# Kernel optimization log

Hardware: AMD Instinct MI355X
Metric: run time of the kernel (lower is better)

The kernel has to match this reference:

```python
import jax, jax.numpy as jnp
import numpy as np

N, M, E, C, F, K = 10000, 20000, 160000, 128, 128, 3
R_CORRECTION = 1.0  # UpsampleModule passes 1 to DPOConv


def setup_inputs() -> dict:
    key = jax.random.key(0)
    ks = jax.random.split(key, 8)
    x = jax.random.normal(ks[0], (N, C), dtype=jnp.float32)
    pos = jax.random.uniform(ks[1], (N, 2), dtype=jnp.float32)
    pos_skip = jax.random.uniform(ks[2], (M, 2), dtype=jnp.float32)
    edge_index = jax.random.randint(ks[3], (2, E), 0, N, dtype=jnp.int64)
    W_conv = jax.random.normal(ks[4], (4 * C, F), dtype=jnp.float32) * 0.02
    b_conv = jnp.zeros((F,), dtype=jnp.float32)
    W2 = jax.random.normal(ks[5], (F, F), dtype=jnp.float32) * 0.02
    b2 = jnp.zeros((F,), dtype=jnp.float32)
    return {"x": x, "pos": pos, "pos_skip": pos_skip, "edge_index": edge_index,
            "W_conv": W_conv, "b_conv": b_conv, "W2": W2, "b2": b2}


def _dpo_conv(x, pos, edge_index, W_conv, b_conv):
    src, dst = edge_index[0], edge_index[1]  # PyG flow: j=source, i=target
    v_j, v_i = x[src], x[dst]                # [E, C]
    diff = pos[dst] - pos[src]               # pos_i - pos_j, [E, 2]
    r2 = jnp.sum(diff * diff, axis=-1)       # [E]
    scale = R_CORRECTION / (r2 + 0.01)       # [E]
    dx = diff[:, 0] * scale
    dy = diff[:, 1] * scale
    v_diff = v_i - v_j
    f = jnp.concatenate([v_diff * dx[:, None], v_diff * dy[:, None], v_j], axis=1)  # [E, 3C]
    agg = jax.ops.segment_sum(f, dst, num_segments=N)
    cnt = jax.ops.segment_sum(jnp.ones((E,), x.dtype), dst, num_segments=N)
    agg = agg / jnp.maximum(cnt, 1.0)[:, None]  # aggr='mean'
    h = jnp.concatenate([agg, x], axis=1) @ W_conv + b_conv  # [N, F]
    return h


def _knn_interpolate(h, pos, pos_skip, k):
    # squared distances target->source, [M, N]
    d2 = jnp.sum((pos_skip[:, None, :] - pos[None, :, :]) ** 2, axis=-1)
    neg_d, idx = jax.lax.top_k(-d2, k)         # k nearest, [M, k]
    w = 1.0 / jnp.maximum(-neg_d, 1e-16)       # inverse squared-distance weights
    return jnp.sum(w[:, :, None] * h[idx], axis=1) / jnp.sum(w, axis=1)[:, None]


def reference(x, pos, pos_skip, edge_index, W_conv, b_conv, W2, b2):
    h = _dpo_conv(x, pos, edge_index, W_conv, b_conv)
    h = jax.nn.elu(h)
    h = jax.nn.elu(h @ W2 + b2)
    return _knn_interpolate(h, pos, pos_skip, K)  # [M, F]
```

## Files before the change

kernel.cpp:

```cpp
#include <hip/hip_runtime.h>
#include <hip/hip_bf16.h>
#include <math.h>
#include <float.h>
#include <stdint.h>

#define N_NODES 10000
#define M_PTS   20000
#define E_EDGES 160000
#define C_CH    128
#define F_CH    128
#define G_GRID  64
#define N_CELLS (G_GRID*G_GRID)
#define NPB     16
#define ECAP    64
#define CCAP    24
#define AROWS   10048
#define GROWS   64
#define S_STRIDE 136
#define N_TILES (N_NODES / NPB)
#define W1SZ (4*C_CH*F_CH)
#define W2SZ (F_CH*F_CH)

typedef __attribute__((ext_vector_type(8))) short short8;
typedef __attribute__((ext_vector_type(4))) float f32x4;

__device__ inline ushort f2bf(float v) {
    __hip_bfloat16 b = __float2bfloat16(v);
    return *reinterpret_cast<ushort*>(&b);
}
__device__ inline float bf2f(ushort u) {
    __hip_bfloat16 b = *reinterpret_cast<__hip_bfloat16*>(&u);
    return __bfloat162float(b);
}
__device__ inline float eluf(float v) { return (v > 0.f) ? v : expm1f(v); }
__device__ inline void insert3(uint64_t key, uint64_t& k0, uint64_t& k1, uint64_t& k2) {
    bool lt2 = key < k2, lt1 = key < k1, lt0 = key < k0;
    k2 = lt1 ? k1 : (lt2 ? key : k2);
    k1 = lt0 ? k0 : (lt1 ? key : k1);
    k0 = lt0 ? key : k0;
}

__global__ __launch_bounds__(256) void build_kernel(const int* __restrict__ ei,
    const float* __restrict__ pos, int* __restrict__ ecur, int* __restrict__ ccur,
    int4* __restrict__ edata, int4* __restrict__ cdata,
    const float* __restrict__ Wc, const float* __restrict__ W2,
    ushort* __restrict__ Wct_h, ushort* __restrict__ Wct_l,
    ushort* __restrict__ W2t_h, ushort* __restrict__ W2t_l)
{
    int i = blockIdx.x * 256 + threadIdx.x;
    if (i < E_EDGES) {
        int src = ei[i];
        int dst = ei[E_EDGES + i];
        float dxv = pos[2*dst]     - pos[2*src];
        float dyv = pos[2*dst + 1] - pos[2*src + 1];
        float r2 = dxv*dxv + dyv*dyv;
        float scale = 1.0f / (r2 + 0.01f);
        int slot = atomicAdd(&ecur[dst], 1);
        if (slot < ECAP)
            edata[dst*ECAP + slot] = make_int4(src, __float_as_int(dxv*scale),
                                               __float_as_int(dyv*scale), 0);
    } else if (i < E_EDGES + N_NODES) {
        int j = i - E_EDGES;
        float px = pos[2*j], py = pos[2*j+1];
        int cx = min(max((int)(px * G_GRID), 0), G_GRID - 1);
        int cy = min(max((int)(py * G_GRID), 0), G_GRID - 1);
        int c = cy * G_GRID + cx;
        int slot = atomicAdd(&ccur[c], 1);
        if (slot < CCAP)
            cdata[c*CCAP + slot] = make_int4(__float_as_int(px), __float_as_int(py), j, 0);
    } else if (i < E_EDGES + N_NODES + W1SZ) {
        int j = i - (E_EDGES + N_NODES);
        int n = j >> 9, k = j & 511;
        float v = Wc[k*F_CH + n];
        ushort h = f2bf(v);
        Wct_h[j] = h;
        Wct_l[j] = f2bf(v - bf2f(h));
    } else if (i < E_EDGES + N_NODES + W1SZ + W2SZ) {
        int j = i - (E_EDGES + N_NODES + W1SZ);
        int n = j >> 7, k = j & 127;
        float v = W2[k*F_CH + n];
        ushort h = f2bf(v);
        W2t_h[j] = h;
        W2t_l[j] = f2bf(v - bf2f(h));
    }
}

__global__ __launch_bounds__(1024, 8) void mega_kernel(const float* __restrict__ x,
    const int* __restrict__ ecur, const int4* __restrict__ edata,
    ushort* __restrict__ Ah, ushort* __restrict__ Al,
    const float* __restrict__ pos_skip, const int* __restrict__ ccur,
    const int4* __restrict__ cdata,
    int* __restrict__ knn_idx, float* __restrict__ knn_w)
{
    const int bid = blockIdx.x;
    const int tid = threadIdx.x;
    const int lane = tid & 63;
    const int wave = tid >> 6;

    if (bid % 5 == 4) {
        int gt = (bid / 5) * 1024 + tid;
        if (gt >= M_PTS * 8) return;
        int t = gt >> 3;
        int sub = gt & 7;
        float tx = pos_skip[2*t], ty = pos_skip[2*t+1];
        const float h = 1.0f / G_GRID;
        int cx = min(max((int)(tx * G_GRID), 0), G_GRID - 1);
        int cy = min(max((int)(ty * G_GRID), 0), G_GRID - 1);

        uint64_t m0 = UINT64_MAX, m1 = UINT64_MAX, m2 = UINT64_MAX;
        bool done;
        {
            uint64_t k0 = UINT64_MAX, k1 = UINT64_MAX, k2 = UINT64_MAX;
            int cc[4];
            int qq[4];
            #pragma unroll
            for (int s = 0; s < 4; s++) {
                int cidx = sub + 8*s;
                int yy = cy + cidx / 5 - 2;
                int xx = cx + cidx % 5 - 2;
                bool ok = (cidx < 25) && (yy >= 0) && (yy < G_GRID) &&
                          (xx >= 0) && (xx < G_GRID);
                cc[s] = ok ? (yy * G_GRID + xx) : -1;
            }
            #pragma unroll
            for (int s = 0; s < 4; s++)
                qq[s] = (cc[s] >= 0) ? min(ccur[cc[s]], CCAP) : 0;
            #pragma unroll
            for (int s = 0; s < 4; s++) {
                const int4* cb = cdata + (size_t)(cc[s] < 0 ? 0 : cc[s]) * CCAP;
                int q = qq[s];
                int p = 0;
                for (; p + 1 < q; p += 2) {
                    int4 sa = cb[p];
                    int4 sb = cb[p+1];
                    float dax = __fadd_rn(__int_as_float(sa.x), -tx);
                    float day = __fadd_rn(__int_as_float(sa.y), -ty);
                    float da  = __fadd_rn(__fmul_rn(dax, dax), __fmul_rn(day, day));
                    insert3(((uint64_t)__float_as_uint(da) << 32) | (uint32_t)sa.z, k0, k1, k2);
                    float dbx = __fadd_rn(__int_as_float(sb.x), -tx);
                    float dby = __fadd_rn(__int_as_float(sb.y), -ty);
                    float db  = __fadd_rn(__fmul_rn(dbx, dbx), __fmul_rn(dby, dby));
                    insert3(((uint64_t)__float_as_uint(db) << 32) | (uint32_t)sb.z, k0, k1, k2);
                }
                if (p < q) {
                    int4 sa = cb[p];
                    float dax = __fadd_rn(__int_as_float(sa.x), -tx);
                    float day = __fadd_rn(__int_as_float(sa.y), -ty);
                    float da  = __fadd_rn(__fmul_rn(dax, dax), __fmul_rn(day, day));
                    insert3(((uint64_t)__float_as_uint(da) << 32) | (uint32_t)sa.z, k0, k1, k2);
                }
            }
            m0 = k0; m1 = k1; m2 = k2;
            #pragma unroll
            for (int m = 1; m <= 4; m <<= 1) {
                uint64_t p0 = __shfl_xor((unsigned long long)m0, m, 64);
                uint64_t p1 = __shfl_xor((unsigned long long)m1, m, 64);
                uint64_t p2 = __shfl_xor((unsigned long long)m2, m, 64);
                insert3(p0, m0, m1, m2);
                insert3(p1, m0, m1, m2);
                insert3(p2, m0, m1, m2);
            }
            float d2cur = __uint_as_float((uint32_t)(m2 >> 32));
            done = (d2cur < (2.0f * h) * (2.0f * h) * 0.99999f);
        }

        if (!done) {
            uint64_t k0 = UINT64_MAX, k1 = UINT64_MAX, k2 = UINT64_MAX;
            m0 = UINT64_MAX; m1 = UINT64_MAX; m2 = UINT64_MAX;
            for (int r = 0; ; r++) {
                if (r >= 2) {
                    m0 = k0; m1 = k1; m2 = k2;
                    #pragma unroll
                    for (int m = 1; m <= 4; m <<= 1) {
                        uint64_t p0 = __shfl_xor((unsigned long long)m0, m, 64);
                        uint64_t p1 = __shfl_xor((unsigned long long)m1, m, 64);
                        uint64_t p2 = __shfl_xor((unsigned long long)m2, m, 64);
                        insert3(p0, m0, m1, m2);
                        insert3(p1, m0, m1, m2);
                        insert3(p2, m0, m1, m2);
                    }
                    float bound = ((r - 1) * h) * ((r - 1) * h) * 0.99999f;
                    float d2cur = __uint_as_float((uint32_t)(m2 >> 32));
                    if (d2cur < bound || r >= G_GRID) break;
                }
                int x0 = max(cx - r, 0), x1 = min(cx + r, G_GRID - 1);
                int y0 = max(cy - r, 0), y1 = min(cy + r, G_GRID - 1);
                int cidx = 0;
                for (int yy = y0; yy <= y1; yy++) {
                    bool yedge = (yy == cy - r) || (yy == cy + r);
                    for (int xx = x0; xx <= x1; xx++) {
                        if (r > 0 && !yedge && xx != cx - r && xx != cx + r) continue;
                        if ((cidx++ & 7) != sub) continue;
                        int c = yy * G_GRID + xx;
                        int pc = min(ccur[c], CCAP);
                        const int4* cb = cdata + c*CCAP;
                        for (int p = 0; p < pc; p++) {
                            int4 sp = cb[p];
                            float ddx = __fadd_rn(__int_as_float(sp.x), -tx);
                            float ddy = __fadd_rn(__int_as_float(sp.y), -ty);
                            float dd = __fadd_rn(__fmul_rn(ddx, ddx), __fmul_rn(ddy, ddy));
                            uint64_t key = ((uint64_t)__float_as_uint(dd) << 32) | (uint32_t)sp.z;
                            insert3(key, k0, k1, k2);
                        }
                    }
                }
            }
        }

        if (sub == 0) {
            float d0 = __uint_as_float((uint32_t)(m0 >> 32));
            float d1 = __uint_as_float((uint32_t)(m1 >> 32));
            float d2 = __uint_as_float((uint32_t)(m2 >> 32));
            float w0 = 1.0f / fmaxf(d0, 1e-16f);
            float w1 = 1.0f / fmaxf(d1, 1e-16f);
            float w2 = 1.0f / fmaxf(d2, 1e-16f);
            float wsum = w0 + w1 + w2;
            knn_idx[t*3+0] = (int)(uint32_t)m0;
            knn_idx[t*3+1] = (int)(uint32_t)m1;
            knn_idx[t*3+2] = (int)(uint32_t)m2;
            knn_w[t*3+0] = w0 / wsum;
            knn_w[t*3+1] = w1 / wsum;
            knn_w[t*3+2] = w2 / wsum;
        }
        return;
    }

    const int agg_id = bid - bid / 5;
    if (agg_id >= N_TILES) return;
    const int nodeBase = agg_id * NPB;
    const float2* xv = (const float2*)x;

    {
        const int rr = wave;
        int node = nodeBase + rr;
        float2 xi = xv[(size_t)node*64 + lane];
        int cnt = ecur[node];
        int m = min(cnt, ECAP);
        int4 er = make_int4(0, 0, 0, 0);
        if (lane < m)
            er = edata[(size_t)node*ECAP + lane];
        double a1x = 0., a1y = 0., a2x = 0., a2y = 0., a3x = 0., a3y = 0.;
        int p = 0;
        for (; p + 7 < m; p += 8) {
            int s0 = __shfl(er.x, p);     int s1 = __shfl(er.x, p+1);
            int s2 = __shfl(er.x, p+2);   int s3 = __shfl(er.x, p+3);
            int s4 = __shfl(er.x, p+4);   int s5 = __shfl(er.x, p+5);
            int s6 = __shfl(er.x, p+6);   int s7 = __shfl(er.x, p+7);
            float dx0 = __int_as_float(__shfl(er.y, p));
            float dy0 = __int_as_float(__shfl(er.z, p));
            float dx1 = __int_as_float(__shfl(er.y, p+1));
            float dy1 = __int_as_float(__shfl(er.z, p+1));
            float dx2 = __int_as_float(__shfl(er.y, p+2));
            float dy2 = __int_as_float(__shfl(er.z, p+2));
            float dx3 = __int_as_float(__shfl(er.y, p+3));
            float dy3 = __int_as_float(__shfl(er.z, p+3));
            float dx4 = __int_as_float(__shfl(er.y, p+4));
            float dy4 = __int_as_float(__shfl(er.z, p+4));
            float dx5 = __int_as_float(__shfl(er.y, p+5));
            float dy5 = __int_as_float(__shfl(er.z, p+5));
            float dx6 = __int_as_float(__shfl(er.y, p+6));
            float dy6 = __int_as_float(__shfl(er.z, p+6));
            float dx7 = __int_as_float(__shfl(er.y, p+7));
            float dy7 = __int_as_float(__shfl(er.z, p+7));
            float2 x0 = xv[(size_t)s0*64 + lane];
            float2 x1 = xv[(size_t)s1*64 + lane];
            float2 x2 = xv[(size_t)s2*64 + lane];
            float2 x3 = xv[(size_t)s3*64 + lane];
            float2 x4 = xv[(size_t)s4*64 + lane];
            float2 x5 = xv[(size_t)s5*64 + lane];
            float2 x6 = xv[(size_t)s6*64 + lane];
            float2 x7 = xv[(size_t)s7*64 + lane];
            a1x += (double)((xi.x-x0.x)*dx0); a1y += (double)((xi.y-x0.y)*dx0);
            a2x += (double)((xi.x-x0.x)*dy0); a2y += (double)((xi.y-x0.y)*dy0);
            a3x += (double)x0.x;              a3y += (double)x0.y;
            a1x += (double)((xi.x-x1.x)*dx1); a1y += (double)((xi.y-x1.y)*dx1);
            a2x += (double)((xi.x-x1.x)*dy1); a2y += (double)((xi.y-x1.y)*dy1);
            a3x += (double)x1.x;              a3y += (double)x1.y;
            a1x += (double)((xi.x-x2.x)*dx2); a1y += (double)((xi.y-x2.y)*dx2);
            a2x += (double)((xi.x-x2.x)*dy2); a2y += (double)((xi.y-x2.y)*dy2);
            a3x += (double)x2.x;              a3y += (double)x2.y;
            a1x += (double)((xi.x-x3.x)*dx3); a1y += (double)((xi.y-x3.y)*dx3);
            a2x += (double)((xi.x-x3.x)*dy3); a2y += (double)((xi.y-x3.y)*dy3);
            a3x += (double)x3.x;              a3y += (double)x3.y;
            a1x += (double)((xi.x-x4.x)*dx4); a1y += (double)((xi.y-x4.y)*dx4);
            a2x += (double)((xi.x-x4.x)*dy4); a2y += (double)((xi.y-x4.y)*dy4);
            a3x += (double)x4.x;              a3y += (double)x4.y;
            a1x += (double)((xi.x-x5.x)*dx5); a1y += (double)((xi.y-x5.y)*dx5);
            a2x += (double)((xi.x-x5.x)*dy5); a2y += (double)((xi.y-x5.y)*dy5);
            a3x += (double)x5.x;              a3y += (double)x5.y;
            a1x += (double)((xi.x-x6.x)*dx6); a1y += (double)((xi.y-x6.y)*dx6);
            a2x += (double)((xi.x-x6.x)*dy6); a2y += (double)((xi.y-x6.y)*dy6);
            a3x += (double)x6.x;              a3y += (double)x6.y;
            a1x += (double)((xi.x-x7.x)*dx7); a1y += (double)((xi.y-x7.y)*dx7);
            a2x += (double)((xi.x-x7.x)*dy7); a2y += (double)((xi.y-x7.y)*dy7);
            a3x += (double)x7.x;              a3y += (double)x7.y;
        }
        for (; p + 3 < m; p += 4) {
            int s0 = __shfl(er.x, p);     int s1 = __shfl(er.x, p+1);
            int s2 = __shfl(er.x, p+2);   int s3 = __shfl(er.x, p+3);
            float dx0 = __int_as_float(__shfl(er.y, p));
            float dy0 = __int_as_float(__shfl(er.z, p));
            float dx1 = __int_as_float(__shfl(er.y, p+1));
            float dy1 = __int_as_float(__shfl(er.z, p+1));
            float dx2 = __int_as_float(__shfl(er.y, p+2));
            float dy2 = __int_as_float(__shfl(er.z, p+2));
            float dx3 = __int_as_float(__shfl(er.y, p+3));
            float dy3 = __int_as_float(__shfl(er.z, p+3));
            float2 x0 = xv[(size_t)s0*64 + lane];
            float2 x1 = xv[(size_t)s1*64 + lane];
            float2 x2 = xv[(size_t)s2*64 + lane];
            float2 x3 = xv[(size_t)s3*64 + lane];
            a1x += (double)((xi.x-x0.x)*dx0); a1y += (double)((xi.y-x0.y)*dx0);
            a2x += (double)((xi.x-x0.x)*dy0); a2y += (double)((xi.y-x0.y)*dy0);
            a3x += (double)x0.x;              a3y += (double)x0.y;
            a1x += (double)((xi.x-x1.x)*dx1); a1y += (double)((xi.y-x1.y)*dx1);
            a2x += (double)((xi.x-x1.x)*dy1); a2y += (double)((xi.y-x1.y)*dy1);
            a3x += (double)x1.x;              a3y += (double)x1.y;
            a1x += (double)((xi.x-x2.x)*dx2); a1y += (double)((xi.y-x2.y)*dx2);
            a2x += (double)((xi.x-x2.x)*dy2); a2y += (double)((xi.y-x2.y)*dy2);
            a3x += (double)x2.x;              a3y += (double)x2.y;
            a1x += (double)((xi.x-x3.x)*dx3); a1y += (double)((xi.y-x3.y)*dx3);
            a2x += (double)((xi.x-x3.x)*dy3); a2y += (double)((xi.y-x3.y)*dy3);
            a3x += (double)x3.x;              a3y += (double)x3.y;
        }
        for (; p < m; p++) {
            int s = __shfl(er.x, p);
            float dxe = __int_as_float(__shfl(er.y, p));
            float dye = __int_as_float(__shfl(er.z, p));
            float2 xj = xv[(size_t)s*64 + lane];
            float vx = xi.x - xj.x, vy = xi.y - xj.y;
            a1x += (double)(vx*dxe); a1y += (double)(vy*dxe);
            a2x += (double)(vx*dye); a2y += (double)(vy*dye);
            a3x += (double)xj.x;     a3y += (double)xj.y;
        }
        float inv = 1.0f / fmaxf((float)cnt, 1.0f);
        float vals[4][2] = {{(float)a1x*inv, (float)a1y*inv},
                            {(float)a2x*inv, (float)a2y*inv},
                            {(float)a3x*inv, (float)a3y*inv},
                            {xi.x, xi.y}};
        uint* Ah32 = (uint*)Ah;
        uint* Al32 = (uint*)Al;
        size_t b32 = (size_t)node*256;
        #pragma unroll
        for (int seg = 0; seg < 4; seg++) {
            ushort hx = f2bf(vals[seg][0]), hy = f2bf(vals[seg][1]);
            ushort lx = f2bf(vals[seg][0] - bf2f(hx)), ly = f2bf(vals[seg][1] - bf2f(hy));
            Ah32[b32 + seg*64 + lane] = (uint)hx | ((uint)hy << 16);
            Al32[b32 + seg*64 + lane] = (uint)lx | ((uint)ly << 16);
        }
    }
}

__global__ __launch_bounds__(512) void gemm_kernel(
    const ushort* __restrict__ Ah, const ushort* __restrict__ Al,
    const ushort* __restrict__ Wct_h, const ushort* __restrict__ Wct_l,
    const ushort* __restrict__ W2t_h, const ushort* __restrict__ W2t_l,
    const float* __restrict__ bc, const float* __restrict__ b2,
    float* __restrict__ h2out)
{
    __shared__ alignas(16) ushort sP0[GROWS * S_STRIDE];
    __shared__ alignas(16) ushort sP1[GROWS * S_STRIDE];

    const int tid   = threadIdx.x;
    const int lane  = tid & 63;
    const int wave  = tid >> 6;
    const int col16 = lane & 15;
    const int quad  = lane >> 4;
    const int ncol  = wave*16 + col16;
    const int rowBase = blockIdx.x * GROWS;

    const float bcv = bc[ncol];
    f32x4 acc0 = {0,0,0,0}, acc1 = {0,0,0,0}, acc2 = {0,0,0,0}, acc3 = {0,0,0,0};

    const int srow = tid >> 3;
    const int sseg = tid & 7;

    for (int kc = 0; kc < 4; kc++) {
        if (kc) __syncthreads();
        {
            size_t g = (size_t)(rowBase + srow)*512 + kc*128 + sseg*16;
            int l = srow*S_STRIDE + sseg*16;
            *(short8*)&sP0[l]     = *(const short8*)&Ah[g];
            *(short8*)&sP0[l + 8] = *(const short8*)&Ah[g + 8];
            *(short8*)&sP1[l]     = *(const short8*)&Al[g];
            *(short8*)&sP1[l + 8] = *(const short8*)&Al[g + 8];
        }
        __syncthreads();
        for (int ks = 0; ks < 4; ks++) {
            int kb = ks*32 + quad*8;
            short8 bh = *(const short8*)(Wct_h + (size_t)ncol*512 + kc*128 + kb);
            short8 bl = *(const short8*)(Wct_l + (size_t)ncol*512 + kc*128 + kb);
            #pragma unroll
            for (int rt = 0; rt < 4; rt++) {
                int ar = (rt*16 + col16)*S_STRIDE + kb;
                short8 ah = *(const short8*)&sP0[ar];
                short8 al = *(const short8*)&sP1[ar];
                f32x4 a = (rt==0)?acc0:(rt==1)?acc1:(rt==2)?acc2:acc3;
                a = __builtin_amdgcn_mfma_f32_16x16x32_bf16(ah, bh, a, 0, 0, 0);
                a = __builtin_amdgcn_mfma_f32_16x16x32_bf16(ah, bl, a, 0, 0, 0);
                a = __builtin_amdgcn_mfma_f32_16x16x32_bf16(al, bh, a, 0, 0, 0);
                if (rt==0) acc0 = a; else if (rt==1) acc1 = a; else if (rt==2) acc2 = a; else acc3 = a;
            }
        }
    }
    __syncthreads();

    #pragma unroll
    for (int rt = 0; rt < 4; rt++) {
        f32x4 a = (rt==0)?acc0:(rt==1)?acc1:(rt==2)?acc2:acc3;
        #pragma unroll
        for (int r = 0; r < 4; r++) {
            int row = rt*16 + quad*4 + r;
            float v = eluf(a[r] + bcv);
            ushort hh = f2bf(v);
            sP0[row*S_STRIDE + ncol] = hh;
            sP1[row*S_STRIDE + ncol] = f2bf(v - bf2f(hh));
        }
    }
    __syncthreads();

    const float b2v = b2[ncol];
    f32x4 c0 = {0,0,0,0}, c1 = {0,0,0,0}, c2 = {0,0,0,0}, c3 = {0,0,0,0};
    for (int ks = 0; ks < 4; ks++) {
        int kb = ks*32 + quad*8;
        short8 bh = *(const short8*)(W2t_h + ncol*128 + kb);
        short8 bl = *(const short8*)(W2t_l + ncol*128 + kb);
        #pragma unroll
        for (int rt = 0; rt < 4; rt++) {
            int ar = (rt*16 + col16)*S_STRIDE + kb;
            short8 ah = *(const short8*)&sP0[ar];
            short8 al = *(const short8*)&sP1[ar];
            f32x4 a = (rt==0)?c0:(rt==1)?c1:(rt==2)?c2:c3;
            a = __builtin_amdgcn_mfma_f32_16x16x32_bf16(ah, bh, a, 0, 0, 0);
            a = __builtin_amdgcn_mfma_f32_16x16x32_bf16(ah, bl, a, 0, 0, 0);
            a = __builtin_amdgcn_mfma_f32_16x16x32_bf16(al, bh, a, 0, 0, 0);
            if (rt==0) c0 = a; else if (rt==1) c1 = a; else if (rt==2) c2 = a; else c3 = a;
        }
    }
    #pragma unroll
    for (int rt = 0; rt < 4; rt++) {
        f32x4 a = (rt==0)?c0:(rt==1)?c1:(rt==2)?c2:c3;
        #pragma unroll
        for (int r = 0; r < 4; r++) {
            int node = rowBase + rt*16 + quad*4 + r;
            if (node < N_NODES)
                h2out[(size_t)node*F_CH + ncol] = eluf(a[r] + b2v);
        }
    }
}

__global__ __launch_bounds__(256) void gather_kernel(const float* __restrict__ h2,
    const int* __restrict__ knn_idx, const float* __restrict__ knn_w,
    float* __restrict__ out)
{
    int m = blockIdx.x * 4 + (threadIdx.x >> 6);
    int lane = threadIdx.x & 63;
    const float2* h2v = (const float2*)h2;
    int j0 = knn_idx[m*3+0], j1 = knn_idx[m*3+1], j2 = knn_idx[m*3+2];
    float w0 = knn_w[m*3+0], w1 = knn_w[m*3+1], w2 = knn_w[m*3+2];
    float2 a = h2v[(size_t)j0*64 + lane], b = h2v[(size_t)j1*64 + lane], c = h2v[(size_t)j2*64 + lane];
    float2 v;
    v.x = w0*a.x + w1*b.x + w2*c.x;
    v.y = w0*a.y + w1*b.y + w2*c.y;
    ((float2*)out)[(size_t)m*64 + lane] = v;
}

extern "C" void kernel_launch(void* const* d_in, const int* in_sizes, int n_in,
                              void* d_out, int out_size, void* d_ws, size_t ws_size,
                              hipStream_t stream) {
    const float* x        = (const float*)d_in[0];
    const float* pos      = (const float*)d_in[1];
    const float* pos_skip = (const float*)d_in[2];
    const int*   ei       = (const int*)  d_in[3];
    const float* Wc       = (const float*)d_in[4];
    const float* bc       = (const float*)d_in[5];
    const float* W2       = (const float*)d_in[6];
    const float* b2       = (const float*)d_in[7];
    float* out = (float*)d_out;

    char* ws = (char*)d_ws;
    size_t off = 0;
    auto alloc = [&](size_t bytes) {
        void* p = ws + off;
        off = (off + bytes + 255) & ~(size_t)255;
        return p;
    };
    int*    ecur    = (int*)   alloc((size_t)N_NODES * 4);
    int*    ccur    = (int*)   alloc((size_t)N_CELLS * 4);
    size_t  cur_bytes = (size_t)((char*)ccur - (char*)ecur) + (size_t)N_CELLS * 4;
    int4*   edata   = (int4*)  alloc((size_t)N_NODES * ECAP * 16);
    int4*   cdata   = (int4*)  alloc((size_t)N_CELLS * CCAP * 16);
    float*  h2      = (float*) alloc((size_t)N_NODES * F_CH * 4);
    int*    knn_idx = (int*)   alloc((size_t)M_PTS * 3 * 4);
    float*  knn_w   = (float*) alloc((size_t)M_PTS * 3 * 4);
    ushort* Wct_h   = (ushort*)alloc((size_t)F_CH * 512 * 2);
    ushort* Wct_l   = (ushort*)alloc((size_t)F_CH * 512 * 2);
    ushort* W2t_h   = (ushort*)alloc((size_t)F_CH * 128 * 2);
    ushort* W2t_l   = (ushort*)alloc((size_t)F_CH * 128 * 2);
    ushort* Ah      = (ushort*)alloc((size_t)AROWS * 512 * 2);
    ushort* Al      = (ushort*)alloc((size_t)AROWS * 512 * 2);

    hipMemsetAsync(ecur, 0, cur_bytes, stream);
    const int TOT = E_EDGES + N_NODES + W1SZ + W2SZ;
    build_kernel<<<(TOT + 255) / 256, 256, 0, stream>>>(ei, pos, ecur, ccur, edata, cdata,
                                                        Wc, W2, Wct_h, Wct_l, W2t_h, W2t_l);
    mega_kernel<<<785, 1024, 0, stream>>>(x, ecur, edata, Ah, Al,
        pos_skip, ccur, cdata, knn_idx, knn_w);
    gemm_kernel<<<(AROWS / GROWS), 512, 0, stream>>>(Ah, Al, Wct_h, Wct_l, W2t_h, W2t_l,
                                                     bc, b2, h2);
    gather_kernel<<<M_PTS / 4, 256, 0, stream>>>(h2, knn_idx, knn_w, out);
}
```

Before: 140.7 us.

## Use 32 lanes per kNN query and interleave kNN and aggregation blocks 1:1

The kNN branch of the fused kernel now gives each query point 32 threads, with one thread per cell of the 5x5 neighbourhood, instead of 8 threads each scanning up to 4 cells. The butterfly top-3 merge grows from 3 to 5 shuffle stages. Blocks alternate one-to-one between kNN and aggregation, so the grid becomes 1250 blocks. This shortens each thread's serial cell scan and balances the two block types better, at the cost of 7 idle lanes per group, more shuffle work and more kNN blocks overall.

```diff
diff --git a/kernel.cpp b/kernel.cpp
--- a/kernel.cpp
+++ b/kernel.cpp
@@ -18,6 +18,8 @@
 #define GROWS   64
 #define S_STRIDE 136
 #define N_TILES (N_NODES / NPB)
+#define KNN_CHUNK 32
+#define N_KNNBLK (M_PTS / KNN_CHUNK)
 #define W1SZ (4*C_CH*F_CH)
 #define W2SZ (F_CH*F_CH)
 
@@ -97,11 +99,10 @@
     const int lane = tid & 63;
     const int wave = tid >> 6;
 
-    if (bid % 5 == 4) {
-        int gt = (bid / 5) * 1024 + tid;
-        if (gt >= M_PTS * 8) return;
-        int t = gt >> 3;
-        int sub = gt & 7;
+    if (bid & 1) {
+        const int grp = tid >> 5;
+        const int sub = tid & 31;
+        const int t = (bid >> 1) * KNN_CHUNK + grp;
         float tx = pos_skip[2*t], ty = pos_skip[2*t+1];
         const float h = 1.0f / G_GRID;
         int cx = min(max((int)(tx * G_GRID), 0), G_GRID - 1);
@@ -111,48 +112,40 @@
         bool done;
         {
             uint64_t k0 = UINT64_MAX, k1 = UINT64_MAX, k2 = UINT64_MAX;
-            int cc[4];
-            int qq[4];
-            #pragma unroll
-            for (int s = 0; s < 4; s++) {
-                int cidx = sub + 8*s;
-                int yy = cy + cidx / 5 - 2;
-                int xx = cx + cidx % 5 - 2;
-                bool ok = (cidx < 25) && (yy >= 0) && (yy < G_GRID) &&
-                          (xx >= 0) && (xx < G_GRID);
-                cc[s] = ok ? (yy * G_GRID + xx) : -1;
+            int q = 0;
+            const int4* cb = cdata;
+            if (sub < 25) {
+                int yy = cy + sub / 5 - 2;
+                int xx = cx + sub % 5 - 2;
+                if (yy >= 0 && yy < G_GRID && xx >= 0 && xx < G_GRID) {
+                    int c = yy * G_GRID + xx;
+                    q = min(ccur[c], CCAP);
+                    cb = cdata + (size_t)c * CCAP;
+                }
             }
-            #pragma unroll
-            for (int s = 0; s < 4; s++)
-                qq[s] = (cc[s] >= 0) ? min(ccur[cc[s]], CCAP) : 0;
-            #pragma unroll
-            for (int s = 0; s < 4; s++) {
-                const int4* cb = cdata + (size_t)(cc[s] < 0 ? 0 : cc[s]) * CCAP;
-                int q = qq[s];
-                int p = 0;
-                for (; p + 1 < q; p += 2) {
-                    int4 sa = cb[p];
-                    int4 sb = cb[p+1];
-                    float dax = __fadd_rn(__int_as_float(sa.x), -tx);
-                    float day = __fadd_rn(__int_as_float(sa.y), -ty);
-                    float da  = __fadd_rn(__fmul_rn(dax, dax), __fmul_rn(day, day));
-                    insert3(((uint64_t)__float_as_uint(da) << 32) | (uint32_t)sa.z, k0, k1, k2);
-                    float dbx = __fadd_rn(__int_as_float(sb.x), -tx);
-                    float dby = __fadd_rn(__int_as_float(sb.y), -ty);
-                    float db  = __fadd_rn(__fmul_rn(dbx, dbx), __fmul_rn(dby, dby));
-                    insert3(((uint64_t)__float_as_uint(db) << 32) | (uint32_t)sb.z, k0, k1, k2);
-                }
-                if (p < q) {
-                    int4 sa = cb[p];
-                    float dax = __fadd_rn(__int_as_float(sa.x), -tx);
-                    float day = __fadd_rn(__int_as_float(sa.y), -ty);
-                    float da  = __fadd_rn(__fmul_rn(dax, dax), __fmul_rn(day, day));
-                    insert3(((uint64_t)__float_as_uint(da) << 32) | (uint32_t)sa.z, k0, k1, k2);
-                }
+            int p = 0;
+            for (; p + 1 < q; p += 2) {
+                int4 sa = cb[p];
+                int4 sb = cb[p+1];
+                float dax = __fadd_rn(__int_as_float(sa.x), -tx);
+                float day = __fadd_rn(__int_as_float(sa.y), -ty);
+                float da  = __fadd_rn(__fmul_rn(dax, dax), __fmul_rn(day, day));
+                insert3(((uint64_t)__float_as_uint(da) << 32) | (uint32_t)sa.z, k0, k1, k2);
+                float dbx = __fadd_rn(__int_as_float(sb.x), -tx);
+                float dby = __fadd_rn(__int_as_float(sb.y), -ty);
+                float db  = __fadd_rn(__fmul_rn(dbx, dbx), __fmul_rn(dby, dby));
+                insert3(((uint64_t)__float_as_uint(db) << 32) | (uint32_t)sb.z, k0, k1, k2);
+            }
+            if (p < q) {
+                int4 sa = cb[p];
+                float dax = __fadd_rn(__int_as_float(sa.x), -tx);
+                float day = __fadd_rn(__int_as_float(sa.y), -ty);
+                float da  = __fadd_rn(__fmul_rn(dax, dax), __fmul_rn(day, day));
+                insert3(((uint64_t)__float_as_uint(da) << 32) | (uint32_t)sa.z, k0, k1, k2);
             }
             m0 = k0; m1 = k1; m2 = k2;
             #pragma unroll
-            for (int m = 1; m <= 4; m <<= 1) {
+            for (int m = 1; m <= 16; m <<= 1) {
                 uint64_t p0 = __shfl_xor((unsigned long long)m0, m, 64);
                 uint64_t p1 = __shfl_xor((unsigned long long)m1, m, 64);
                 uint64_t p2 = __shfl_xor((unsigned long long)m2, m, 64);
@@ -171,7 +164,7 @@
                 if (r >= 2) {
                     m0 = k0; m1 = k1; m2 = k2;
                     #pragma unroll
-                    for (int m = 1; m <= 4; m <<= 1) {
+                    for (int m = 1; m <= 16; m <<= 1) {
                         uint64_t p0 = __shfl_xor((unsigned long long)m0, m, 64);
                         uint64_t p1 = __shfl_xor((unsigned long long)m1, m, 64);
                         uint64_t p2 = __shfl_xor((unsigned long long)m2, m, 64);
@@ -190,7 +183,7 @@
                     bool yedge = (yy == cy - r) || (yy == cy + r);
                     for (int xx = x0; xx <= x1; xx++) {
                         if (r > 0 && !yedge && xx != cx - r && xx != cx + r) continue;
-                        if ((cidx++ & 7) != sub) continue;
+                        if ((cidx++ & 31) != sub) continue;
                         int c = yy * G_GRID + xx;
                         int pc = min(ccur[c], CCAP);
                         const int4* cb = cdata + c*CCAP;
@@ -225,7 +218,7 @@
         return;
     }
 
-    const int agg_id = bid - bid / 5;
+    const int agg_id = bid >> 1;
     if (agg_id >= N_TILES) return;
     const int nodeBase = agg_id * NPB;
     const float2* xv = (const float2*)x;
@@ -504,7 +497,7 @@
     const int TOT = E_EDGES + N_NODES + W1SZ + W2SZ;
     build_kernel<<<(TOT + 255) / 256, 256, 0, stream>>>(ei, pos, ecur, ccur, edata, cdata,
                                                         Wc, W2, Wct_h, Wct_l, W2t_h, W2t_l);
-    mega_kernel<<<785, 1024, 0, stream>>>(x, ecur, edata, Ah, Al,
+    mega_kernel<<<2 * N_TILES, 1024, 0, stream>>>(x, ecur, edata, Ah, Al,
         pos_skip, ccur, cdata, knn_idx, knn_w);
     gemm_kernel<<<(AROWS / GROWS), 512, 0, stream>>>(Ah, Al, Wct_h, Wct_l, W2t_h, W2t_l,
                                                      bc, b2, h2);
```

After: 138.7 us. About the same (-1.4%).
